# Kernel optimization log

Measured on AMD Instinct MI355X. Metric: run time of the kernel, lower is better.

The kernel has to match this reference:

```python
import jax, jax.numpy as jnp
import numpy as np

N, E = 50000, 800000
IN, HID, OUT = 128, 128, 64
BN_EPS = 1e-5


def _w(key, fan_in, fan_out):
    return jax.random.normal(key, (fan_in, fan_out), dtype=jnp.float32) / np.sqrt(fan_in)


def setup_inputs() -> dict:
    key = jax.random.key(0)
    ks = jax.random.split(key, 12)
    x = jax.random.normal(ks[0], (N, IN), dtype=jnp.float32)
    src = jax.random.randint(ks[1], (E,), 0, N, dtype=jnp.int32)
    dst = jax.random.randint(ks[2], (E,), 0, N, dtype=jnp.int32)
    eps = jax.random.normal(ks[3], (N, OUT), dtype=jnp.float32)
    return {
        "x": x, "src": src, "dst": dst, "eps": eps,
        # SAGEConv 1: in -> hidden (lin_l has bias, lin_r no bias, mean aggr)
        "W1l": _w(ks[4], IN, HID), "W1r": _w(ks[5], IN, HID), "b1": jnp.zeros((HID,), jnp.float32),
        "g1": jnp.ones((HID,), jnp.float32), "be1": jnp.zeros((HID,), jnp.float32),
        # SAGEConv 2: hidden -> 2*hidden
        "W2l": _w(ks[6], HID, 2 * HID), "W2r": _w(ks[7], HID, 2 * HID), "b2": jnp.zeros((2 * HID,), jnp.float32),
        "g2": jnp.ones((2 * HID,), jnp.float32), "be2": jnp.zeros((2 * HID,), jnp.float32),
        # SAGEConv 3: 2*hidden -> 2*out
        "W3l": _w(ks[8], 2 * HID, 2 * OUT), "W3r": _w(ks[9], 2 * HID, 2 * OUT), "b3": jnp.zeros((2 * OUT,), jnp.float32),
    }


def _sage(h, src, dst, Wl, Wr, b):
    # mean-aggregate source features at destination nodes, then two GEMMs
    msg = jax.ops.segment_sum(h[src], dst, num_segments=N)          # [N, F]
    deg = jax.ops.segment_sum(jnp.ones((src.shape[0],), h.dtype), dst, num_segments=N)
    aggr = msg / jnp.maximum(deg, 1.0)[:, None]
    return aggr @ Wl + h @ Wr + b


def _bn(h, gamma, beta):
    m = jnp.mean(h, axis=0)
    v = jnp.var(h, axis=0)
    return gamma * (h - m) * jax.lax.rsqrt(v + BN_EPS) + beta


def reference(x, src, dst, eps, W1l, W1r, b1, g1, be1, W2l, W2r, b2, g2, be2, W3l, W3r, b3):
    h = jax.nn.relu(_sage(x, src, dst, W1l, W1r, b1))
    h = _bn(h, g1, be1)                       # dropout = identity (eval)
    h = jax.nn.relu(_sage(h, src, dst, W2l, W2r, b2))
    h = _bn(h, g2, be2)
    h = _sage(h, src, dst, W3l, W3r, b3)      # [N, 2*OUT]
    mean, log_std = jnp.split(h, 2, axis=-1)
    z = mean + jnp.exp(log_std) * eps         # reparameterize
    return z
```

## Files before the change

### kernel.cpp

```cpp
#include <hip/hip_runtime.h>
#include <math.h>

#define N_NODES 50000
#define N_EDGES 800000
#define BN_EPS_F 1e-5f
#define SCAN_BS 512
#define SCAN_NB 98
#define RC2 196
#define RQ2 25
#define GXP2 200

typedef unsigned short ushort_t;
typedef unsigned int uint_t;
typedef __attribute__((ext_vector_type(8))) short bf16x8;
typedef __attribute__((ext_vector_type(4))) float f32x4;

static __device__ __forceinline__ float4 ld4(const float* p) {
    return *reinterpret_cast<const float4*>(p);
}
static __device__ __forceinline__ float bf2f(ushort_t u) {
    return __uint_as_float(((uint_t)u) << 16);
}
static __device__ __forceinline__ ushort_t f2b(float f) {
    uint_t u = __float_as_uint(f);
    u += 0x7fffu + ((u >> 16) & 1u);
    return (ushort_t)(u >> 16);
}


__global__ void k_zero_i32(int* __restrict__ p, int n) {
    int i = blockIdx.x * blockDim.x + threadIdx.x;
    if (i < n) p[i] = 0;
}

__global__ void k_pre(const int* __restrict__ dst, int* __restrict__ deg2,
                      ushort_t* __restrict__ rank,
                      const float* __restrict__ x, ushort_t* __restrict__ xb,
                      const float* __restrict__ W1l, const float* __restrict__ W1r,
                      const float* __restrict__ W2l, ushort_t* __restrict__ wt1l,
                      ushort_t* __restrict__ wt1r, ushort_t* __restrict__ wt2l) {
    int b = blockIdx.x;
    if (b < 6250) {
        int role = b & 1;
        int id = (b >> 1) * 256 + threadIdx.x;
        if (role == 0) {
            rank[id] = (ushort_t)atomicAdd(&deg2[dst[id] * 16], 1);
        } else {
            float4 a = ld4(x + (size_t)id * 8);
            float4 c = ld4(x + (size_t)id * 8 + 4);
            uint_t o0 = (uint_t)f2b(a.x) | ((uint_t)f2b(a.y) << 16);
            uint_t o1 = (uint_t)f2b(a.z) | ((uint_t)f2b(a.w) << 16);
            uint_t o2 = (uint_t)f2b(c.x) | ((uint_t)f2b(c.y) << 16);
            uint_t o3 = (uint_t)f2b(c.z) | ((uint_t)f2b(c.w) << 16);
            *reinterpret_cast<uint4*>(xb + (size_t)id * 8) = make_uint4(o0, o1, o2, o3);
        }
    } else {
        int idx = (b - 6250) * 256 + threadIdx.x;
        if (idx < 16384) {
            int f = idx >> 7, k = idx & 127;
            wt1l[idx] = f2b(W1l[(size_t)k * 128 + f]);
        } else if (idx < 32768) {
            int j = idx - 16384;
            int f = j >> 7, k = j & 127;
            wt1r[j] = f2b(W1r[(size_t)k * 128 + f]);
        } else {
            int j = idx - 32768;
            int f = j >> 7, k = j & 127;
            wt2l[j] = f2b(W2l[(size_t)k * 256 + f]);
        }
    }
}

__global__ void k_scan1(const int* __restrict__ deg2, int* __restrict__ offs, int* __restrict__ bsum) {
    __shared__ int sh[SCAN_BS];
    int t = threadIdx.x;
    int g = blockIdx.x * SCAN_BS + t;
    int v = (g < N_NODES) ? deg2[g * 16] : 0;
    sh[t] = v;
    __syncthreads();
    for (int off = 1; off < SCAN_BS; off <<= 1) {
        int add = (t >= off) ? sh[t - off] : 0;
        __syncthreads();
        sh[t] += add;
        __syncthreads();
    }
    if (g < N_NODES) offs[g] = sh[t] - v;
    if (t == SCAN_BS - 1) bsum[blockIdx.x] = sh[t];
}

__global__ void k_scan2(int* __restrict__ bsum, int nb) {
    __shared__ int sh[128];
    int t = threadIdx.x;
    int v = (t < nb) ? bsum[t] : 0;
    sh[t] = v;
    __syncthreads();
    for (int off = 1; off < 128; off <<= 1) {
        int add = (t >= off) ? sh[t - off] : 0;
        __syncthreads();
        sh[t] += add;
        __syncthreads();
    }
    if (t < nb) bsum[t] = sh[t] - v;
}

__global__ void k_scan3(const int* __restrict__ deg2, int* __restrict__ offs,
                        const int* __restrict__ bsum, float* __restrict__ inv_deg,
                        int* __restrict__ degc) {
    int g = blockIdx.x * blockDim.x + threadIdx.x;
    if (g < N_NODES) {
        offs[g] += bsum[g / SCAN_BS];
        int d = deg2[g * 16];
        degc[g] = d;
        inv_deg[g] = 1.0f / (float)(d > 1 ? d : 1);
    }
}

__global__ void k_fill2(const int* __restrict__ src, const int* __restrict__ dst,
                        const int* __restrict__ offs, const ushort_t* __restrict__ rank,
                        ushort_t* __restrict__ eids) {
    int e = blockIdx.x * blockDim.x + threadIdx.x;
    if (e < N_EDGES) eids[offs[dst[e]] + (int)rank[e]] = (ushort_t)src[e];
}


__global__ void k_prep2(const float* __restrict__ W2r, const float* __restrict__ b2,
                        const float* __restrict__ scsh1, ushort_t* __restrict__ wt2r,
                        float* __restrict__ bias2) {
    int bid = blockIdx.x;
    if (bid < 128) {
        int idx = bid * 256 + threadIdx.x;
        int f = idx >> 7, k = idx & 127;
        wt2r[idx] = f2b(scsh1[k] * W2r[(size_t)k * 256 + f]);
    } else {
        int f = threadIdx.x;
        float s = b2[f];
        for (int k = 0; k < 128; ++k) s += scsh1[128 + k] * W2r[(size_t)k * 256 + f];
        bias2[f] = s;
    }
}

__global__ void k_prep3(const float* __restrict__ W3l, const float* __restrict__ W3r,
                        const float* __restrict__ b3, const float* __restrict__ scsh2,
                        ushort_t* __restrict__ wt3l, ushort_t* __restrict__ wt3r,
                        float* __restrict__ bias3l, float* __restrict__ bias3r) {
    int bid = blockIdx.x;
    if (bid < 256) {
        int half = bid >> 7;
        int idx = (bid & 127) * 256 + threadIdx.x;
        int f = idx >> 8, k = idx & 255;
        const float* W = half ? W3r : W3l;
        ushort_t* WT = half ? wt3r : wt3l;
        WT[idx] = f2b(scsh2[k] * W[(size_t)k * 128 + f]);
    } else {
        int t = threadIdx.x;
        int f = t & 127;
        const float* W = (t < 128) ? W3l : W3r;
        float s = (t < 128) ? 0.f : b3[f];
        for (int k = 0; k < 256; ++k) s += scsh2[256 + k] * W[(size_t)k * 128 + f];
        float* out = (t < 128) ? bias3l : bias3r;
        out[f] = s;
    }
}


#define ACCUM8(a) do { \
    acc[0] += bf2f((ushort_t)(a).x); acc[1] += bf2f((ushort_t)((a).x >> 16)); \
    acc[2] += bf2f((ushort_t)(a).y); acc[3] += bf2f((ushort_t)((a).y >> 16)); \
    acc[4] += bf2f((ushort_t)(a).z); acc[5] += bf2f((ushort_t)((a).z >> 16)); \
    acc[6] += bf2f((ushort_t)(a).w); acc[7] += bf2f((ushort_t)((a).w >> 16)); } while (0)

static __device__ __forceinline__ void gather_rows_g(
        const ushort_t* __restrict__ h, const ushort_t* __restrict__ eids,
        int beg, int d, size_t coff, float* acc) {
    int j = 0;
    for (; j + 8 <= d; j += 8) {
        uint4 a[8];
#pragma unroll
        for (int k = 0; k < 8; ++k) {
            int s = eids[beg + j + k];
            a[k] = *reinterpret_cast<const uint4*>(h + (size_t)s * 128 + coff);
        }
#pragma unroll
        for (int k = 0; k < 8; ++k) ACCUM8(a[k]);
    }
    for (; j + 4 <= d; j += 4) {
        uint4 a[4];
#pragma unroll
        for (int k = 0; k < 4; ++k) {
            int s = eids[beg + j + k];
            a[k] = *reinterpret_cast<const uint4*>(h + (size_t)s * 128 + coff);
        }
#pragma unroll
        for (int k = 0; k < 4; ++k) ACCUM8(a[k]);
    }
    for (; j + 2 <= d; j += 2) {
        int s0 = eids[beg + j];
        int s1 = eids[beg + j + 1];
        uint4 a = *reinterpret_cast<const uint4*>(h + (size_t)s0 * 128 + coff);
        uint4 b = *reinterpret_cast<const uint4*>(h + (size_t)s1 * 128 + coff);
        ACCUM8(a); ACCUM8(b);
    }
    if (j < d) {
        int s0 = eids[beg + j];
        uint4 a = *reinterpret_cast<const uint4*>(h + (size_t)s0 * 128 + coff);
        ACCUM8(a);
    }
}

template<int BN>
__global__ __launch_bounds__(256) void k_agg16(
        const ushort_t* __restrict__ h, const ushort_t* __restrict__ eids,
        const int* __restrict__ offs, const int* __restrict__ deg,
        const float* __restrict__ inv_deg, const float* __restrict__ scsh,
        ushort_t* __restrict__ out) {
    const int node = blockIdx.x * 16 + (threadIdx.x >> 4);
    const int lr = threadIdx.x & 15;
    if (node >= N_NODES) return;
    float acc[8];
#pragma unroll
    for (int v = 0; v < 8; ++v) acc[v] = 0.f;
    const int beg = offs[node];
    const int d = deg[node];
    const size_t coff = (size_t)lr * 8;
    gather_rows_g(h, eids, beg, d, coff, acc);

    float sc = inv_deg[node];
    if (BN) {
        float4 sa0 = ld4(&scsh[lr * 8]), sa1 = ld4(&scsh[lr * 8 + 4]);
        float4 sb0 = ld4(&scsh[128 + lr * 8]), sb1 = ld4(&scsh[128 + lr * 8 + 4]);
        if (d > 0) {
            acc[0] = acc[0] * sc * sa0.x + sb0.x; acc[1] = acc[1] * sc * sa0.y + sb0.y;
            acc[2] = acc[2] * sc * sa0.z + sb0.z; acc[3] = acc[3] * sc * sa0.w + sb0.w;
            acc[4] = acc[4] * sc * sa1.x + sb1.x; acc[5] = acc[5] * sc * sa1.y + sb1.y;
            acc[6] = acc[6] * sc * sa1.z + sb1.z; acc[7] = acc[7] * sc * sa1.w + sb1.w;
        } else {
#pragma unroll
            for (int v = 0; v < 8; ++v) acc[v] = 0.f;
        }
    } else {
#pragma unroll
        for (int v = 0; v < 8; ++v) acc[v] *= sc;
    }
    uint4 o;
    o.x = (uint_t)f2b(acc[0]) | ((uint_t)f2b(acc[1]) << 16);
    o.y = (uint_t)f2b(acc[2]) | ((uint_t)f2b(acc[3]) << 16);
    o.z = (uint_t)f2b(acc[4]) | ((uint_t)f2b(acc[5]) << 16);
    o.w = (uint_t)f2b(acc[6]) | ((uint_t)f2b(acc[7]) << 16);
    *reinterpret_cast<uint4*>(out + (size_t)node * 128 + coff) = o;
}

__global__ __launch_bounds__(256) void k_agg_reparam(
        const ushort_t* __restrict__ t3, const ushort_t* __restrict__ eids,
        const int* __restrict__ offs, const int* __restrict__ deg,
        const float* __restrict__ inv_deg, const ushort_t* __restrict__ u,
        const float* __restrict__ eps, float* __restrict__ z) {
    const int node = blockIdx.x * 16 + (threadIdx.x >> 4);
    const int lr = threadIdx.x & 15;
    if (node >= N_NODES) return;
    float acc[8];
#pragma unroll
    for (int v = 0; v < 8; ++v) acc[v] = 0.f;
    const int beg = offs[node];
    const int d = deg[node];
    const size_t coff = (size_t)lr * 8;
    gather_rows_g(t3, eids, beg, d, coff, acc);
    float ls[8];
#pragma unroll
    for (int v = 0; v < 8; ++v) ls[v] = __shfl_down(acc[v], 8);

    if (lr < 8) {
        float sc = inv_deg[node];
        uint4 um4 = *reinterpret_cast<const uint4*>(u + (size_t)node * 128 + lr * 8);
        uint4 ul4 = *reinterpret_cast<const uint4*>(u + (size_t)node * 128 + 64 + lr * 8);
        const float* ep = eps + (size_t)node * 64 + lr * 8;
        float4 e0 = ld4(ep), e1 = ld4(ep + 4);
        float um[8], ul[8];
        um[0] = bf2f((ushort_t)um4.x); um[1] = bf2f((ushort_t)(um4.x >> 16));
        um[2] = bf2f((ushort_t)um4.y); um[3] = bf2f((ushort_t)(um4.y >> 16));
        um[4] = bf2f((ushort_t)um4.z); um[5] = bf2f((ushort_t)(um4.z >> 16));
        um[6] = bf2f((ushort_t)um4.w); um[7] = bf2f((ushort_t)(um4.w >> 16));
        ul[0] = bf2f((ushort_t)ul4.x); ul[1] = bf2f((ushort_t)(ul4.x >> 16));
        ul[2] = bf2f((ushort_t)ul4.y); ul[3] = bf2f((ushort_t)(ul4.y >> 16));
        ul[4] = bf2f((ushort_t)ul4.z); ul[5] = bf2f((ushort_t)(ul4.z >> 16));
        ul[6] = bf2f((ushort_t)ul4.w); ul[7] = bf2f((ushort_t)(ul4.w >> 16));
        float4 o0, o1;
        o0.x = (acc[0] * sc + um[0]) + expf(ls[0] * sc + ul[0]) * e0.x;
        o0.y = (acc[1] * sc + um[1]) + expf(ls[1] * sc + ul[1]) * e0.y;
        o0.z = (acc[2] * sc + um[2]) + expf(ls[2] * sc + ul[2]) * e0.z;
        o0.w = (acc[3] * sc + um[3]) + expf(ls[3] * sc + ul[3]) * e0.w;
        o1.x = (acc[4] * sc + um[4]) + expf(ls[4] * sc + ul[4]) * e1.x;
        o1.y = (acc[5] * sc + um[5]) + expf(ls[5] * sc + ul[5]) * e1.y;
        o1.z = (acc[6] * sc + um[6]) + expf(ls[6] * sc + ul[6]) * e1.z;
        o1.w = (acc[7] * sc + um[7]) + expf(ls[7] * sc + ul[7]) * e1.w;
        float* zp = z + (size_t)node * 64 + lr * 8;
        *reinterpret_cast<float4*>(zp) = o0;
        *reinterpret_cast<float4*>(zp + 4) = o1;
    }
}


template<int RELU, int DUAL, int STATS, int SEL3, int K>
__global__ __launch_bounds__(256, 2) void k_gemm_direct(
        const ushort_t* __restrict__ A1, const ushort_t* __restrict__ A2,
        const ushort_t* __restrict__ B1, const ushort_t* __restrict__ B2,
        const float* __restrict__ bias, ushort_t* __restrict__ out,
        int F, float* __restrict__ partials,
        const float* __restrict__ bias2, ushort_t* __restrict__ out2) {
    const int bid = blockIdx.x;
    const int grp = bid >> 3;
    const int y = grp / RQ2;
    const int rq = grp - y * RQ2;
    const int r = (bid & 7) + (rq << 3);
    if (r >= RC2) return;
    const int row0 = r * 256;

    int colblk = y, outsel = 0;
    if (SEL3) { colblk = y & 1; outsel = y >> 1; }
    const int col0 = colblk * 64;
    const ushort_t* __restrict__ Bp = (SEL3 && outsel) ? B2 : B1;
    const float* __restrict__ biasp = (SEL3 && outsel) ? bias2 : bias;
    ushort_t* __restrict__ outp = (SEL3 && outsel) ? out2 : out;

    const int tid = threadIdx.x;
    const int lane = tid & 63;
    const int w = tid >> 6;
    const int q = lane >> 4, lr = lane & 15;
    const int wrow = row0 + w * 64;

    int arow[4];
#pragma unroll
    for (int mf = 0; mf < 4; ++mf) {
        int rr = wrow + mf * 16 + lr;
        arow[mf] = rr < N_NODES ? rr : N_NODES - 1;
    }

    f32x4 acc[4][4];
#pragma unroll
    for (int mf = 0; mf < 4; ++mf)
#pragma unroll
        for (int nf = 0; nf < 4; ++nf)
            acc[mf][nf] = (f32x4){0.f, 0.f, 0.f, 0.f};

#pragma unroll
    for (int m = 0; m < (DUAL ? 2 : 1); ++m) {
        const ushort_t* __restrict__ A = m ? A2 : A1;
        const ushort_t* __restrict__ B = m ? B2 : Bp;
#pragma unroll
        for (int kh = 0; kh < K / 128; ++kh) {
            const int kb = kh * 128;
            bf16x8 av[4][4], bv[4][4];
#pragma unroll
            for (int k0 = 0; k0 < 4; ++k0) {
#pragma unroll
                for (int f = 0; f < 4; ++f) {
                    av[k0][f] = *reinterpret_cast<const bf16x8*>(
                        A + (size_t)arow[f] * K + kb + k0 * 32 + q * 8);
                    bv[k0][f] = *reinterpret_cast<const bf16x8*>(
                        B + (size_t)(col0 + f * 16 + lr) * K + kb + k0 * 32 + q * 8);
                }
            }
#pragma unroll
            for (int k0 = 0; k0 < 4; ++k0)
#pragma unroll
                for (int mf = 0; mf < 4; ++mf)
#pragma unroll
                    for (int nf = 0; nf < 4; ++nf)
                        acc[mf][nf] = __builtin_amdgcn_mfma_f32_16x16x32_bf16(
                            av[k0][mf], bv[k0][nf], acc[mf][nf], 0, 0, 0);
        }
    }

    __shared__ __align__(16) short lw[4][64][68];
    __shared__ float sdf[2][16][64];

    float s[4], s2[4];
#pragma unroll
    for (int nf = 0; nf < 4; ++nf) { s[nf] = 0.f; s2[nf] = 0.f; }
#pragma unroll
    for (int nf = 0; nf < 4; ++nf) {
        float bvs = biasp[col0 + nf * 16 + lr];
#pragma unroll
        for (int mf = 0; mf < 4; ++mf) {
#pragma unroll
            for (int b = 0; b < 4; ++b) {
                int rrow = mf * 16 + q * 4 + b;
                float v = acc[mf][nf][b] + bvs;
                if (RELU) v = fmaxf(v, 0.f);
                if (STATS && (wrow + rrow) < N_NODES) { s[nf] += v; s2[nf] += v * v; }
                lw[w][rrow][nf * 16 + lr] = (short)f2b(v);
            }
        }
    }
#pragma unroll
    for (int rr = 0; rr < 8; ++rr) {
        int row = rr * 8 + (lane >> 3);
        int gr = wrow + row;
        if (gr < N_NODES) {
            uint4 vv = *reinterpret_cast<const uint4*>(&lw[w][row][(lane & 7) * 8]);
            *reinterpret_cast<uint4*>(outp + (size_t)gr * F + col0 + (lane & 7) * 8) = vv;
        }
    }

    if constexpr (STATS) {
        const int u = w * 4 + q;
#pragma unroll
        for (int nf = 0; nf < 4; ++nf) {
            sdf[0][u][nf * 16 + lr] = s[nf];
            sdf[1][u][nf * 16 + lr] = s2[nf];
        }
        __syncthreads();
        if (tid < 64) {
            float ss = 0.f, qq = 0.f;
#pragma unroll
            for (int u2 = 0; u2 < 16; ++u2) {
                ss += sdf[0][u2][tid];
                qq += sdf[1][u2][tid];
            }
            int cg = col0 + tid;
            partials[(size_t)cg * GXP2 + r] = ss;
            partials[(size_t)(F + cg) * GXP2 + r] = qq;
        }
    }
}


template<int F>
__global__ __launch_bounds__(64) void k_bn_scsh(
        const float* __restrict__ partials, const float* __restrict__ gamma,
        const float* __restrict__ beta, float* __restrict__ scsh) {
    const int c = blockIdx.x;
    const int l = threadIdx.x;
    float s = 0.f, q2 = 0.f;
    for (int g = l; g < RC2; g += 64) {
        s += partials[(size_t)c * GXP2 + g];
        q2 += partials[(size_t)(F + c) * GXP2 + g];
    }
#pragma unroll
    for (int off = 1; off < 64; off <<= 1) {
        s += __shfl_xor(s, off);
        q2 += __shfl_xor(q2, off);
    }
    if (l == 0) {
        float mean = s * (1.0f / N_NODES);
        float var = q2 * (1.0f / N_NODES) - mean * mean;
        float sc = gamma[c] * rsqrtf(var + BN_EPS_F);
        scsh[c] = sc;
        scsh[F + c] = beta[c] - mean * sc;
    }
}


extern "C" void kernel_launch(void* const* d_in, const int* in_sizes, int n_in,
                              void* d_out, int out_size, void* d_ws, size_t ws_size,
                              hipStream_t stream) {
    (void)in_sizes; (void)n_in; (void)out_size; (void)ws_size;
    const float* x   = (const float*)d_in[0];
    const int*   src = (const int*)d_in[1];
    const int*   dst = (const int*)d_in[2];
    const float* eps = (const float*)d_in[3];
    const float* W1l = (const float*)d_in[4];
    const float* W1r = (const float*)d_in[5];
    const float* b1  = (const float*)d_in[6];
    const float* g1  = (const float*)d_in[7];
    const float* be1 = (const float*)d_in[8];
    const float* W2l = (const float*)d_in[9];
    const float* W2r = (const float*)d_in[10];
    const float* b2  = (const float*)d_in[11];
    const float* g2  = (const float*)d_in[12];
    const float* be2 = (const float*)d_in[13];
    const float* W3l = (const float*)d_in[14];
    const float* W3r = (const float*)d_in[15];
    const float* b3  = (const float*)d_in[16];
    float* z = (float*)d_out;

    char* ws = (char*)d_ws;
    size_t off = 0;
    auto alloc = [&](size_t bytes) -> char* {
        char* p = ws + off;
        off += (bytes + 255) & ~(size_t)255;
        return p;
    };
    int*      deg2   = (int*)alloc((size_t)N_NODES * 16 * 4);
    size_t zero_bytes = off;
    ushort_t* rank   = (ushort_t*)alloc((size_t)N_EDGES * 2);
    ushort_t* eids   = (ushort_t*)alloc((size_t)N_EDGES * 2);
    float*    scshs  = (float*)alloc(1024 * 4);
    float*    biases = (float*)alloc(512 * 4);
    int*      offs   = (int*)alloc(N_NODES * 4);
    int*      bsum   = (int*)alloc(128 * 4);
    int*      degc   = (int*)alloc(N_NODES * 4);
    float*    invd   = (float*)alloc(N_NODES * 4);
    ushort_t* xb     = (ushort_t*)alloc((size_t)N_NODES * 128 * 2);
    ushort_t* h1b    = (ushort_t*)alloc((size_t)N_NODES * 128 * 2);
    ushort_t* h2b    = (ushort_t*)alloc((size_t)N_NODES * 256 * 2);
    ushort_t* aggrb  = (ushort_t*)alloc((size_t)N_NODES * 256 * 2);
    ushort_t* u3b    = (ushort_t*)alloc((size_t)N_NODES * 128 * 2);
    float*    parts  = (float*)alloc((size_t)512 * GXP2 * 4);
    ushort_t* wt1l   = (ushort_t*)alloc(128 * 128 * 2);
    ushort_t* wt1r   = (ushort_t*)alloc(128 * 128 * 2);
    ushort_t* wt2l   = (ushort_t*)alloc(256 * 128 * 2);
    ushort_t* wt2r   = (ushort_t*)alloc(256 * 128 * 2);
    ushort_t* wt3l   = (ushort_t*)alloc(128 * 256 * 2);
    ushort_t* wt3r   = (ushort_t*)alloc(128 * 256 * 2);
    ushort_t* t3b    = aggrb;

    float* scsh1  = scshs;
    float* scsh2  = scshs + 256;
    float* bias2  = biases;
    float* bias3l = biases + 256;
    float* bias3r = biases + 384;

    k_zero_i32<<<((int)(zero_bytes / 4) + 255) / 256, 256, 0, stream>>>((int*)ws, (int)(zero_bytes / 4));
    k_pre<<<6506, 256, 0, stream>>>(dst, deg2, rank, x, xb, W1l, W1r, W2l, wt1l, wt1r, wt2l);
    k_scan1<<<SCAN_NB, SCAN_BS, 0, stream>>>(deg2, offs, bsum);
    k_scan2<<<1, 128, 0, stream>>>(bsum, SCAN_NB);
    k_scan3<<<(N_NODES + 255) / 256, 256, 0, stream>>>(deg2, offs, bsum, invd, degc);
    k_fill2<<<(N_EDGES + 255) / 256, 256, 0, stream>>>(src, dst, offs, rank, eids);

    const int AGG_BLKS = N_NODES / 16;

    k_agg16<0><<<AGG_BLKS, 256, 0, stream>>>(xb, eids, offs, degc, invd, nullptr, aggrb);
    k_gemm_direct<1, 1, 1, 0, 128><<<8 * RQ2 * 2, 256, 0, stream>>>(
        aggrb, xb, wt1l, wt1r, b1, h1b, 128, parts, nullptr, nullptr);
    k_bn_scsh<128><<<128, 64, 0, stream>>>(parts, g1, be1, scsh1);

    k_prep2<<<129, 256, 0, stream>>>(W2r, b2, scsh1, wt2r, bias2);
    k_agg16<1><<<AGG_BLKS, 256, 0, stream>>>(h1b, eids, offs, degc, invd, scsh1, aggrb);
    k_gemm_direct<1, 1, 1, 0, 128><<<8 * RQ2 * 4, 256, 0, stream>>>(
        aggrb, h1b, wt2l, wt2r, bias2, h2b, 256, parts, nullptr, nullptr);
    k_bn_scsh<256><<<256, 64, 0, stream>>>(parts, g2, be2, scsh2);

    k_prep3<<<257, 256, 0, stream>>>(W3l, W3r, b3, scsh2, wt3l, wt3r, bias3l, bias3r);
    k_gemm_direct<0, 0, 0, 1, 256><<<8 * RQ2 * 4, 256, 0, stream>>>(
        h2b, nullptr, wt3l, wt3r, bias3l, t3b, 128, nullptr, bias3r, u3b);
    k_agg_reparam<<<AGG_BLKS, 256, 0, stream>>>(t3b, eids, offs, degc, invd, u3b, eps, z);
}
```

Before: 255.5 us.

## Shrink GEMM tiles, fold BN finalize into prep kernels, partition edge fill by dst

Row tiles in the direct GEMM shrink from 256 to 128, with each block's four waves split 2x2 over rows and columns. The K-loop now walks 64-wide slices, and launch bounds ask for 4 blocks per CU, aiming for more blocks and better occupancy. The separate BN scale/shift kernels are removed: each prep kernel now recomputes the scale and shift redundantly in every block from the partial sums, saving two launches at the cost of extra reads of the partials. The edge-fill kernel is also split into 8 destination-range classes per chunk to improve write locality into eids, though every edge is now read 8 times.

Result: slower. 320.3 us (+25.4%).

```diff
diff --git a/kernel.cpp b/kernel.cpp
--- a/kernel.cpp
+++ b/kernel.cpp
@@ -6,9 +6,10 @@
 #define BN_EPS_F 1e-5f
 #define SCAN_BS 512
 #define SCAN_NB 98
-#define RC2 196
-#define RQ2 25
-#define GXP2 200
+#define RC 391
+#define RQ 49
+#define GXP 392
+#define FILL_CH 4096
 
 typedef unsigned short ushort_t;
 typedef unsigned int uint_t;
@@ -115,50 +116,103 @@
     }
 }
 
-__global__ void k_fill2(const int* __restrict__ src, const int* __restrict__ dst,
-                        const int* __restrict__ offs, const ushort_t* __restrict__ rank,
-                        ushort_t* __restrict__ eids) {
-    int e = blockIdx.x * blockDim.x + threadIdx.x;
-    if (e < N_EDGES) eids[offs[dst[e]] + (int)rank[e]] = (ushort_t)src[e];
-}
-
-
-__global__ void k_prep2(const float* __restrict__ W2r, const float* __restrict__ b2,
-                        const float* __restrict__ scsh1, ushort_t* __restrict__ wt2r,
-                        float* __restrict__ bias2) {
-    int bid = blockIdx.x;
+__global__ __launch_bounds__(256) void k_fill3(
+        const int* __restrict__ src, const int* __restrict__ dst,
+        const int* __restrict__ offs, const ushort_t* __restrict__ rank,
+        ushort_t* __restrict__ eids) {
+    const int cls = blockIdx.x & 7;
+    const int chunk = blockIdx.x >> 3;
+    const int lo = cls * (N_NODES / 8);
+    const int hi = lo + (N_NODES / 8);
+    int base = chunk * FILL_CH + threadIdx.x;
+#pragma unroll
+    for (int it = 0; it < FILL_CH / 256; ++it) {
+        int e = base + it * 256;
+        if (e < N_EDGES) {
+            int d = dst[e];
+            if (d >= lo && d < hi)
+                eids[offs[d] + (int)rank[e]] = (ushort_t)src[e];
+        }
+    }
+}
+
+
+__global__ __launch_bounds__(256) void k_prep2(
+        const float* __restrict__ W2r, const float* __restrict__ b2,
+        const float* __restrict__ g1, const float* __restrict__ be1,
+        const float* __restrict__ parts, ushort_t* __restrict__ wt2r,
+        float* __restrict__ bias2, float* __restrict__ scsh1g) {
+    __shared__ float sc[128], sh[128];
+    const int t = threadIdx.x;
+    if (t < 128) {
+        float s = 0.f, q2 = 0.f;
+        const float* ps = parts + (size_t)t * GXP;
+        const float* pq = parts + (size_t)(128 + t) * GXP;
+        for (int g = 0; g + 4 <= RC; g += 4) {
+            float4 a = ld4(ps + g), b = ld4(pq + g);
+            s += a.x + a.y + a.z + a.w;
+            q2 += b.x + b.y + b.z + b.w;
+        }
+        for (int g = RC & ~3; g < RC; ++g) { s += ps[g]; q2 += pq[g]; }
+        float mean = s * (1.0f / N_NODES);
+        float var = q2 * (1.0f / N_NODES) - mean * mean;
+        float scv = g1[t] * rsqrtf(var + BN_EPS_F);
+        sc[t] = scv;
+        sh[t] = be1[t] - mean * scv;
+    }
+    __syncthreads();
+    const int bid = blockIdx.x;
     if (bid < 128) {
-        int idx = bid * 256 + threadIdx.x;
+        int idx = bid * 256 + t;
         int f = idx >> 7, k = idx & 127;
-        wt2r[idx] = f2b(scsh1[k] * W2r[(size_t)k * 256 + f]);
+        wt2r[idx] = f2b(sc[k] * W2r[(size_t)k * 256 + f]);
     } else {
-        int f = threadIdx.x;
-        float s = b2[f];
-        for (int k = 0; k < 128; ++k) s += scsh1[128 + k] * W2r[(size_t)k * 256 + f];
-        bias2[f] = s;
-    }
-}
-
-__global__ void k_prep3(const float* __restrict__ W3l, const float* __restrict__ W3r,
-                        const float* __restrict__ b3, const float* __restrict__ scsh2,
-                        ushort_t* __restrict__ wt3l, ushort_t* __restrict__ wt3r,
-                        float* __restrict__ bias3l, float* __restrict__ bias3r) {
-    int bid = blockIdx.x;
+        float s = b2[t];
+        for (int k = 0; k < 128; ++k) s += sh[k] * W2r[(size_t)k * 256 + t];
+        bias2[t] = s;
+        if (t < 128) { scsh1g[t] = sc[t]; scsh1g[128 + t] = sh[t]; }
+    }
+}
+
+__global__ __launch_bounds__(256) void k_prep3(
+        const float* __restrict__ W3l, const float* __restrict__ W3r,
+        const float* __restrict__ b3, const float* __restrict__ g2,
+        const float* __restrict__ be2, const float* __restrict__ parts,
+        ushort_t* __restrict__ wt3l, ushort_t* __restrict__ wt3r,
+        float* __restrict__ bias3l, float* __restrict__ bias3r) {
+    __shared__ float sc[256], sh[256];
+    const int t = threadIdx.x;
+    {
+        float s = 0.f, q2 = 0.f;
+        const float* ps = parts + (size_t)t * GXP;
+        const float* pq = parts + (size_t)(256 + t) * GXP;
+        for (int g = 0; g + 4 <= RC; g += 4) {
+            float4 a = ld4(ps + g), b = ld4(pq + g);
+            s += a.x + a.y + a.z + a.w;
+            q2 += b.x + b.y + b.z + b.w;
+        }
+        for (int g = RC & ~3; g < RC; ++g) { s += ps[g]; q2 += pq[g]; }
+        float mean = s * (1.0f / N_NODES);
+        float var = q2 * (1.0f / N_NODES) - mean * mean;
+        float scv = g2[t] * rsqrtf(var + BN_EPS_F);
+        sc[t] = scv;
+        sh[t] = be2[t] - mean * scv;
+    }
+    __syncthreads();
+    const int bid = blockIdx.x;
     if (bid < 256) {
         int half = bid >> 7;
-        int idx = (bid & 127) * 256 + threadIdx.x;
+        int idx = (bid & 127) * 256 + t;
         int f = idx >> 8, k = idx & 255;
         const float* W = half ? W3r : W3l;
         ushort_t* WT = half ? wt3r : wt3l;
-        WT[idx] = f2b(scsh2[k] * W[(size_t)k * 128 + f]);
+        WT[idx] = f2b(sc[k] * W[(size_t)k * 128 + f]);
     } else {
-        int t = threadIdx.x;
         int f = t & 127;
         const float* W = (t < 128) ? W3l : W3r;
         float s = (t < 128) ? 0.f : b3[f];
-        for (int k = 0; k < 256; ++k) s += scsh2[256 + k] * W[(size_t)k * 128 + f];
-        float* out = (t < 128) ? bias3l : bias3r;
-        out[f] = s;
+        for (int k = 0; k < 256; ++k) s += sh[k] * W[(size_t)k * 128 + f];
+        ((t < 128) ? bias3l : bias3r)[f] = s;
     }
 }
 
@@ -299,8 +353,8 @@
 }
 
 
-template<int RELU, int DUAL, int STATS, int SEL3, int K>
-__global__ __launch_bounds__(256, 2) void k_gemm_direct(
+template<int RELU, int DUAL, int STATS, int SEL3, int K, int YT>
+__global__ __launch_bounds__(256, 4) void k_gemm_direct(
         const ushort_t* __restrict__ A1, const ushort_t* __restrict__ A2,
         const ushort_t* __restrict__ B1, const ushort_t* __restrict__ B2,
         const float* __restrict__ bias, ushort_t* __restrict__ out,
@@ -308,11 +362,11 @@
         const float* __restrict__ bias2, ushort_t* __restrict__ out2) {
     const int bid = blockIdx.x;
     const int grp = bid >> 3;
-    const int y = grp / RQ2;
-    const int rq = grp - y * RQ2;
+    const int y = grp / RQ;
+    const int rq = grp - y * RQ;
     const int r = (bid & 7) + (rq << 3);
-    if (r >= RC2) return;
-    const int row0 = r * 256;
+    if (r >= RC) return;
+    const int row0 = r * 128;
 
     int colblk = y, outsel = 0;
     if (SEL3) { colblk = y & 1; outsel = y >> 1; }
@@ -325,7 +379,8 @@
     const int lane = tid & 63;
     const int w = tid >> 6;
     const int q = lane >> 4, lr = lane & 15;
-    const int wrow = row0 + w * 64;
+    const int wrow = row0 + (w >> 1) * 64;
+    const int wcol = col0 + (w & 1) * 32;
 
     int arow[4];
 #pragma unroll
@@ -334,11 +389,11 @@
         arow[mf] = rr < N_NODES ? rr : N_NODES - 1;
     }
 
-    f32x4 acc[4][4];
+    f32x4 acc[4][2];
 #pragma unroll
     for (int mf = 0; mf < 4; ++mf)
 #pragma unroll
-        for (int nf = 0; nf < 4; ++nf)
+        for (int nf = 0; nf < 2; ++nf)
             acc[mf][nf] = (f32x4){0.f, 0.f, 0.f, 0.f};
 
 #pragma unroll
@@ -346,106 +401,82 @@
         const ushort_t* __restrict__ A = m ? A2 : A1;
         const ushort_t* __restrict__ B = m ? B2 : Bp;
 #pragma unroll
-        for (int kh = 0; kh < K / 128; ++kh) {
-            const int kb = kh * 128;
-            bf16x8 av[4][4], bv[4][4];
-#pragma unroll
-            for (int k0 = 0; k0 < 4; ++k0) {
-#pragma unroll
-                for (int f = 0; f < 4; ++f) {
+        for (int kh = 0; kh < K / 64; ++kh) {
+            const int kb = kh * 64;
+            bf16x8 av[2][4], bv[2][2];
+#pragma unroll
+            for (int k0 = 0; k0 < 2; ++k0) {
+#pragma unroll
+                for (int f = 0; f < 4; ++f)
                     av[k0][f] = *reinterpret_cast<const bf16x8*>(
                         A + (size_t)arow[f] * K + kb + k0 * 32 + q * 8);
+#pragma unroll
+                for (int f = 0; f < 2; ++f)
                     bv[k0][f] = *reinterpret_cast<const bf16x8*>(
-                        B + (size_t)(col0 + f * 16 + lr) * K + kb + k0 * 32 + q * 8);
-                }
+                        B + (size_t)(wcol + f * 16 + lr) * K + kb + k0 * 32 + q * 8);
             }
 #pragma unroll
-            for (int k0 = 0; k0 < 4; ++k0)
+            for (int k0 = 0; k0 < 2; ++k0)
 #pragma unroll
                 for (int mf = 0; mf < 4; ++mf)
 #pragma unroll
-                    for (int nf = 0; nf < 4; ++nf)
+                    for (int nf = 0; nf < 2; ++nf)
                         acc[mf][nf] = __builtin_amdgcn_mfma_f32_16x16x32_bf16(
                             av[k0][mf], bv[k0][nf], acc[mf][nf], 0, 0, 0);
         }
     }
 
-    __shared__ __align__(16) short lw[4][64][68];
-    __shared__ float sdf[2][16][64];
-
-    float s[4], s2[4];
-#pragma unroll
-    for (int nf = 0; nf < 4; ++nf) { s[nf] = 0.f; s2[nf] = 0.f; }
-#pragma unroll
-    for (int nf = 0; nf < 4; ++nf) {
-        float bvs = biasp[col0 + nf * 16 + lr];
+    __shared__ __align__(16) short lw[4][64][36];
+    __shared__ float sdf[2][8][64];
+
+    float s[2], s2[2];
+#pragma unroll
+    for (int nf = 0; nf < 2; ++nf) { s[nf] = 0.f; s2[nf] = 0.f; }
+#pragma unroll
+    for (int nf = 0; nf < 2; ++nf) {
+        float bvs = biasp[wcol + nf * 16 + lr];
 #pragma unroll
         for (int mf = 0; mf < 4; ++mf) {
 #pragma unroll
             for (int b = 0; b < 4; ++b) {
-                int rrow = mf * 16 + q * 4 + b;
+                int rloc = mf * 16 + q * 4 + b;
                 float v = acc[mf][nf][b] + bvs;
                 if (RELU) v = fmaxf(v, 0.f);
-                if (STATS && (wrow + rrow) < N_NODES) { s[nf] += v; s2[nf] += v * v; }
-                lw[w][rrow][nf * 16 + lr] = (short)f2b(v);
+                if (STATS && (wrow + rloc) < N_NODES) { s[nf] += v; s2[nf] += v * v; }
+                lw[w][rloc][nf * 16 + lr] = (short)f2b(v);
             }
         }
     }
 #pragma unroll
-    for (int rr = 0; rr < 8; ++rr) {
-        int row = rr * 8 + (lane >> 3);
+    for (int it = 0; it < 4; ++it) {
+        int row = it * 16 + (lane >> 2);
         int gr = wrow + row;
         if (gr < N_NODES) {
-            uint4 vv = *reinterpret_cast<const uint4*>(&lw[w][row][(lane & 7) * 8]);
-            *reinterpret_cast<uint4*>(outp + (size_t)gr * F + col0 + (lane & 7) * 8) = vv;
+            uint4 vv = *reinterpret_cast<const uint4*>(&lw[w][row][(lane & 3) * 8]);
+            *reinterpret_cast<uint4*>(outp + (size_t)gr * F + wcol + (lane & 3) * 8) = vv;
         }
     }
 
     if constexpr (STATS) {
-        const int u = w * 4 + q;
-#pragma unroll
-        for (int nf = 0; nf < 4; ++nf) {
-            sdf[0][u][nf * 16 + lr] = s[nf];
-            sdf[1][u][nf * 16 + lr] = s2[nf];
+        const int u = (w >> 1) * 4 + q;
+#pragma unroll
+        for (int nf = 0; nf < 2; ++nf) {
+            int cb = (w & 1) * 32 + nf * 16 + lr;
+            sdf[0][u][cb] = s[nf];
+            sdf[1][u][cb] = s2[nf];
         }
         __syncthreads();
         if (tid < 64) {
             float ss = 0.f, qq = 0.f;
 #pragma unroll
-            for (int u2 = 0; u2 < 16; ++u2) {
+            for (int u2 = 0; u2 < 8; ++u2) {
                 ss += sdf[0][u2][tid];
                 qq += sdf[1][u2][tid];
             }
             int cg = col0 + tid;
-            partials[(size_t)cg * GXP2 + r] = ss;
-            partials[(size_t)(F + cg) * GXP2 + r] = qq;
-        }
-    }
-}
-
-
-template<int F>
-__global__ __launch_bounds__(64) void k_bn_scsh(
-        const float* __restrict__ partials, const float* __restrict__ gamma,
-        const float* __restrict__ beta, float* __restrict__ scsh) {
-    const int c = blockIdx.x;
-    const int l = threadIdx.x;
-    float s = 0.f, q2 = 0.f;
-    for (int g = l; g < RC2; g += 64) {
-        s += partials[(size_t)c * GXP2 + g];
-        q2 += partials[(size_t)(F + c) * GXP2 + g];
-    }
-#pragma unroll
-    for (int off = 1; off < 64; off <<= 1) {
-        s += __shfl_xor(s, off);
-        q2 += __shfl_xor(q2, off);
-    }
-    if (l == 0) {
-        float mean = s * (1.0f / N_NODES);
-        float var = q2 * (1.0f / N_NODES) - mean * mean;
-        float sc = gamma[c] * rsqrtf(var + BN_EPS_F);
-        scsh[c] = sc;
-        scsh[F + c] = beta[c] - mean * sc;
+            partials[(size_t)cg * GXP + r] = ss;
+            partials[(size_t)(F + cg) * GXP + r] = qq;
+        }
     }
 }
 
@@ -484,7 +515,7 @@
     size_t zero_bytes = off;
     ushort_t* rank   = (ushort_t*)alloc((size_t)N_EDGES * 2);
     ushort_t* eids   = (ushort_t*)alloc((size_t)N_EDGES * 2);
-    float*    scshs  = (float*)alloc(1024 * 4);
+    float*    scsh1g = (float*)alloc(256 * 4);
     float*    biases = (float*)alloc(512 * 4);
     int*      offs   = (int*)alloc(N_NODES * 4);
     int*      bsum   = (int*)alloc(128 * 4);
@@ -495,7 +526,7 @@
     ushort_t* h2b    = (ushort_t*)alloc((size_t)N_NODES * 256 * 2);
     ushort_t* aggrb  = (ushort_t*)alloc((size_t)N_NODES * 256 * 2);
     ushort_t* u3b    = (ushort_t*)alloc((size_t)N_NODES * 128 * 2);
-    float*    parts  = (float*)alloc((size_t)512 * GXP2 * 4);
+    float*    parts  = (float*)alloc((size_t)512 * GXP * 4);
     ushort_t* wt1l   = (ushort_t*)alloc(128 * 128 * 2);
     ushort_t* wt1r   = (ushort_t*)alloc(128 * 128 * 2);
     ushort_t* wt2l   = (ushort_t*)alloc(256 * 128 * 2);
@@ -504,8 +535,6 @@
     ushort_t* wt3r   = (ushort_t*)alloc(128 * 256 * 2);
     ushort_t* t3b    = aggrb;
 
-    float* scsh1  = scshs;
-    float* scsh2  = scshs + 256;
     float* bias2  = biases;
     float* bias3l = biases + 256;
     float* bias3r = biases + 384;
@@ -515,23 +544,22 @@
     k_scan1<<<SCAN_NB, SCAN_BS, 0, stream>>>(deg2, offs, bsum);
     k_scan2<<<1, 128, 0, stream>>>(bsum, SCAN_NB);
     k_scan3<<<(N_NODES + 255) / 256, 256, 0, stream>>>(deg2, offs, bsum, invd, degc);
-    k_fill2<<<(N_EDGES + 255) / 256, 256, 0, stream>>>(src, dst, offs, rank, eids);
+    k_fill3<<<8 * ((N_EDGES + FILL_CH - 1) / FILL_CH), 256, 0, stream>>>(src, dst, offs, rank, eids);
 
     const int AGG_BLKS = N_NODES / 16;
+    const int GEMM_G = 8 * RQ;
 
     k_agg16<0><<<AGG_BLKS, 256, 0, stream>>>(xb, eids, offs, degc, invd, nullptr, aggrb);
-    k_gemm_direct<1, 1, 1, 0, 128><<<8 * RQ2 * 2, 256, 0, stream>>>(
+    k_gemm_direct<1, 1, 1, 0, 128, 2><<<GEMM_G * 2, 256, 0, stream>>>(
         aggrb, xb, wt1l, wt1r, b1, h1b, 128, parts, nullptr, nullptr);
-    k_bn_scsh<128><<<128, 64, 0, stream>>>(parts, g1, be1, scsh1);
-
-    k_prep2<<<129, 256, 0, stream>>>(W2r, b2, scsh1, wt2r, bias2);
-    k_agg16<1><<<AGG_BLKS, 256, 0, stream>>>(h1b, eids, offs, degc, invd, scsh1, aggrb);
-    k_gemm_direct<1, 1, 1, 0, 128><<<8 * RQ2 * 4, 256, 0, stream>>>(
+
+    k_prep2<<<129, 256, 0, stream>>>(W2r, b2, g1, be1, parts, wt2r, bias2, scsh1g);
+    k_agg16<1><<<AGG_BLKS, 256, 0, stream>>>(h1b, eids, offs, degc, invd, scsh1g, aggrb);
+    k_gemm_direct<1, 1, 1, 0, 128, 4><<<GEMM_G * 4, 256, 0, stream>>>(
         aggrb, h1b, wt2l, wt2r, bias2, h2b, 256, parts, nullptr, nullptr);
-    k_bn_scsh<256><<<256, 64, 0, stream>>>(parts, g2, be2, scsh2);
-
-    k_prep3<<<257, 256, 0, stream>>>(W3l, W3r, b3, scsh2, wt3l, wt3r, bias3l, bias3r);
-    k_gemm_direct<0, 0, 0, 1, 256><<<8 * RQ2 * 4, 256, 0, stream>>>(
+
+    k_prep3<<<257, 256, 0, stream>>>(W3l, W3r, b3, g2, be2, parts, wt3l, wt3r, bias3l, bias3r);
+    k_gemm_direct<0, 0, 0, 1, 256, 4><<<GEMM_G * 4, 256, 0, stream>>>(
         h2b, nullptr, wt3l, wt3r, bias3l, t3b, 128, nullptr, bias3r, u3b);
     k_agg_reparam<<<AGG_BLKS, 256, 0, stream>>>(t3b, eids, offs, degc, invd, u3b, eps, z);
 }
```
